# Optimization experiments

Hardware: AMD Instinct MI355X
Metric: run time of the kernel (lower is better)

Reference implementation:

```python
import jax, jax.numpy as jnp
import numpy as np

NUM_HEADS = 16

def setup_inputs() -> dict:
    key = jax.random.key(0)
    ks = jax.random.split(key, 7)
    B, S, D = 2, 2048, 1024
    X = jax.random.normal(ks[0], (B, S, D), dtype=jnp.float32)
    s = 1.0 / np.sqrt(D)
    Wq = jax.random.normal(ks[1], (D, D), dtype=jnp.float32) * s
    Wk = jax.random.normal(ks[2], (D, D), dtype=jnp.float32) * s
    Wv = jax.random.normal(ks[3], (D, D), dtype=jnp.float32) * s
    Wo = jax.random.normal(ks[4], (D, D), dtype=jnp.float32) * s
    bo = jnp.zeros((D,), dtype=jnp.float32)
    return {"X": X, "Wq": Wq, "Wk": Wk, "Wv": Wv, "Wo": Wo, "bo": bo}

def reference(X, Wq, Wk, Wv, Wo, bo):
    B, S, D = X.shape
    H = NUM_HEADS
    hd = D // H
    # project and split heads -> [B, H, S, hd]
    def split(t):
        return t.reshape(B, S, H, hd).transpose(0, 2, 1, 3)
    q = split(X @ Wq)
    k = split(X @ Wk)
    v = split(X @ Wv)
    scores = jnp.einsum('bhqd,bhkd->bhqk', q, k) / jnp.sqrt(jnp.float32(hd))
    causal = jnp.tril(jnp.ones((S, S), dtype=bool))
    scores = jnp.where(causal, scores, -jnp.inf)
    weights = jax.nn.softmax(scores, axis=-1)  # dropout p=0 -> identity
    ctx = jnp.einsum('bhqk,bhkd->bhqd', weights, v)
    ctx = ctx.transpose(0, 2, 1, 3).reshape(B, S, D)
    return ctx @ Wo + bo
```

## Files before the change

kernel.cpp:

```cpp
#include <hip/hip_runtime.h>


typedef __attribute__((ext_vector_type(8))) short short8;
typedef __attribute__((ext_vector_type(4))) short short4v;
typedef __attribute__((ext_vector_type(4))) float floatx4;

__device__ inline unsigned short f2bf(float f) {
  unsigned u = __float_as_uint(f);
  unsigned r = (u + 0x7fffu + ((u >> 16) & 1u)) >> 16;
  return (unsigned short)r;
}

__device__ __forceinline__ float fast_exp2(float x) {
#if __has_builtin(__builtin_amdgcn_exp2f)
  return __builtin_amdgcn_exp2f(x);
#else
  float r;
  asm volatile("v_exp_f32_e32 %0, %1" : "=v"(r) : "v"(x));
  return r;
#endif
}

__device__ __forceinline__ void gll16(const unsigned short* g, unsigned short* l) {
  __builtin_amdgcn_global_load_lds(
      (const __attribute__((address_space(1))) unsigned int*)(g),
      (__attribute__((address_space(3))) unsigned int*)(l),
      16, 0, 0);
}

constexpr int B_ = 2, S_ = 2048, D_ = 1024, H_ = 16, HD_ = 64;

__global__ __launch_bounds__(256) void prep_inputs(
    const float* __restrict__ x, unsigned short* __restrict__ xb,
    const float* __restrict__ w0, const float* __restrict__ w1,
    const float* __restrict__ w2, const float* __restrict__ w3,
    unsigned short* __restrict__ wt_base)
{
  if (blockIdx.z == 4) {
    const int tid = threadIdx.y * 32 + threadIdx.x;
    const size_t base =
        ((size_t)(blockIdx.y * 32 + blockIdx.x) * 256 + tid) * 16;
#pragma unroll
    for (int half = 0; half < 2; ++half) {
      const size_t i = base + half * 8;
      float4 a = *(const float4*)(x + i);
      float4 b = *(const float4*)(x + i + 4);
      short8 o;
      o[0] = (short)f2bf(a.x); o[1] = (short)f2bf(a.y);
      o[2] = (short)f2bf(a.z); o[3] = (short)f2bf(a.w);
      o[4] = (short)f2bf(b.x); o[5] = (short)f2bf(b.y);
      o[6] = (short)f2bf(b.z); o[7] = (short)f2bf(b.w);
      *(short8*)(xb + i) = o;
    }
    return;
  }
  const float* src;
  switch (blockIdx.z) {
    case 0: src = w0; break;
    case 1: src = w1; break;
    case 2: src = w2; break;
    default: src = w3; break;
  }
  unsigned short* dst = wt_base + (size_t)blockIdx.z * 1024 * 1024;
  __shared__ unsigned short t[32][33];
  const int bx = blockIdx.x * 32;
  const int by = blockIdx.y * 32;
  const int x_ = threadIdx.x;
  for (int yy = threadIdx.y; yy < 32; yy += 8)
    t[yy][x_] = f2bf(src[(size_t)(by + yy) * 1024 + bx + x_]);
  __syncthreads();
  for (int yy = threadIdx.y; yy < 32; yy += 8)
    dst[(size_t)(bx + yy) * 1024 + by + x_] = t[x_][yy];
}

__global__ __launch_bounds__(256) void gemm256_qkv(
    const unsigned short* __restrict__ A,
    const unsigned short* __restrict__ Bt,
    unsigned short* __restrict__ Qo,
    unsigned short* __restrict__ Ko,
    unsigned short* __restrict__ Vt)
{
  __shared__ unsigned short sA[2][128 * 32];
  __shared__ unsigned short sB[2][128 * 32];
  const int K = 1024;

  const int L = blockIdx.y * 24 + blockIdx.x;
  const int rid = (L & 7) * 96 + (L >> 3);
  const int brow = rid / 24, bcol = rid % 24;
  const int m0 = brow * 128;
  const int bn0 = bcol * 128;

  const int tid = threadIdx.x, wave = tid >> 6, lane = tid & 63;
  const int g = lane >> 4, ml = lane & 15;
  const int wm = wave & 1, wn = wave >> 1;

  const unsigned short* ag0 = A + (size_t)(m0 + (tid >> 2)) * K + (tid & 3) * 8;
  const unsigned short* ag1 = ag0 + (size_t)64 * K;
  const unsigned short* bg0 = Bt + (size_t)(bn0 + (tid >> 2)) * K + (tid & 3) * 8;
  const unsigned short* bg1 = bg0 + (size_t)64 * K;
  const int woff = wave * 512;

  floatx4 acc[4][4];
#pragma unroll
  for (int mt = 0; mt < 4; ++mt)
#pragma unroll
    for (int nt = 0; nt < 4; ++nt) acc[mt][nt] = (floatx4){0.f, 0.f, 0.f, 0.f};

  for (int k0 = 0; k0 < K; k0 += 64) {
    __syncthreads();
#pragma unroll
    for (int t = 0; t < 2; ++t) {
      gll16(ag0 + k0 + t * 32, sA[t] + woff);
      gll16(ag1 + k0 + t * 32, sA[t] + 2048 + woff);
      gll16(bg0 + k0 + t * 32, sB[t] + woff);
      gll16(bg1 + k0 + t * 32, sB[t] + 2048 + woff);
    }
    __syncthreads();
#pragma unroll
    for (int t = 0; t < 2; ++t) {
      short8 af[4], bf[4];
#pragma unroll
      for (int mt = 0; mt < 4; ++mt)
        af[mt] = *(const short8*)(sA[t] + (wm * 64 + mt * 16 + ml) * 32 + g * 8);
#pragma unroll
      for (int nt = 0; nt < 4; ++nt)
        bf[nt] = *(const short8*)(sB[t] + (wn * 64 + nt * 16 + ml) * 32 + g * 8);
#pragma unroll
      for (int mt = 0; mt < 4; ++mt)
#pragma unroll
        for (int nt = 0; nt < 4; ++nt)
          acc[mt][nt] = __builtin_amdgcn_mfma_f32_16x16x32_bf16(
              af[mt], bf[nt], acc[mt][nt], 0, 0, 0);
    }
  }

  const int proj = bcol >> 3;
  const int col0 = (bcol & 7) * 128;
  if (proj < 2) {
    unsigned short* out = (proj == 0) ? Qo : Ko;
#pragma unroll
    for (int mt = 0; mt < 4; ++mt) {
#pragma unroll
      for (int nt = 0; nt < 4; ++nt) {
        const int col = col0 + wn * 64 + nt * 16 + ml;
#pragma unroll
        for (int r = 0; r < 4; ++r) {
          const int row = m0 + wm * 64 + mt * 16 + g * 4 + r;
          out[(size_t)row * 1024 + col] = f2bf(acc[mt][nt][r]);
        }
      }
    }
  } else {
    const int bq = m0 >> 11;
    const int sbase = (m0 & 2047);
#pragma unroll
    for (int mt = 0; mt < 4; ++mt) {
      const int s0 = sbase + wm * 64 + mt * 16 + g * 4;
#pragma unroll
      for (int nt = 0; nt < 4; ++nt) {
        const int col = col0 + wn * 64 + nt * 16 + ml;
        const int h = col >> 6, d = col & 63;
        short4v o;
        o[0] = (short)f2bf(acc[mt][nt][0]);
        o[1] = (short)f2bf(acc[mt][nt][1]);
        o[2] = (short)f2bf(acc[mt][nt][2]);
        o[3] = (short)f2bf(acc[mt][nt][3]);
        *(short4v*)(Vt + ((size_t)((bq * 16 + h) * 64 + d)) * 2048 + s0) = o;
      }
    }
  }
}

__global__ __launch_bounds__(256) void gemm_wo64(
    const unsigned short* __restrict__ A,
    const unsigned short* __restrict__ Bt,
    const float* __restrict__ bias,
    float* __restrict__ C)
{
  __shared__ unsigned short sA[4][64 * 32];
  __shared__ unsigned short sB[4][128 * 32];
  const int K = 1024;

  const int L = blockIdx.y * 8 + blockIdx.x;
  const int rid = (L & 7) * 64 + (L >> 3);
  const int m0 = (rid >> 3) * 64;
  const int bn0 = (rid & 7) * 128;

  const int tid = threadIdx.x, wave = tid >> 6, lane = tid & 63;
  const int g = lane >> 4, ml = lane & 15;
  const int wm = wave & 1, wn = wave >> 1;

  const unsigned short* ag =
      A + (size_t)(m0 + wave * 16 + (lane >> 2)) * K + (lane & 3) * 8;
  const unsigned short* bg0 = Bt + (size_t)(bn0 + (tid >> 2)) * K + (tid & 3) * 8;
  const unsigned short* bg1 = bg0 + (size_t)64 * K;
  const int woff = wave * 512;

  floatx4 acc[2][4];
#pragma unroll
  for (int mt = 0; mt < 2; ++mt)
#pragma unroll
    for (int nt = 0; nt < 4; ++nt) acc[mt][nt] = (floatx4){0.f, 0.f, 0.f, 0.f};

  for (int k0 = 0; k0 < K; k0 += 128) {
    __syncthreads();
#pragma unroll
    for (int t = 0; t < 4; ++t) {
      gll16(ag + k0 + t * 32, sA[t] + woff);
      gll16(bg0 + k0 + t * 32, sB[t] + woff);
      gll16(bg1 + k0 + t * 32, sB[t] + 2048 + woff);
    }
    __syncthreads();
#pragma unroll
    for (int t = 0; t < 4; ++t) {
      short8 af[2], bf[4];
#pragma unroll
      for (int mt = 0; mt < 2; ++mt)
        af[mt] = *(const short8*)(sA[t] + (wm * 32 + mt * 16 + ml) * 32 + g * 8);
#pragma unroll
      for (int nt = 0; nt < 4; ++nt)
        bf[nt] = *(const short8*)(sB[t] + (wn * 64 + nt * 16 + ml) * 32 + g * 8);
#pragma unroll
      for (int mt = 0; mt < 2; ++mt)
#pragma unroll
        for (int nt = 0; nt < 4; ++nt)
          acc[mt][nt] = __builtin_amdgcn_mfma_f32_16x16x32_bf16(
              af[mt], bf[nt], acc[mt][nt], 0, 0, 0);
    }
  }

#pragma unroll
  for (int mt = 0; mt < 2; ++mt) {
#pragma unroll
    for (int nt = 0; nt < 4; ++nt) {
      const int col = bn0 + wn * 64 + nt * 16 + ml;
      const float badd = bias[col];
#pragma unroll
      for (int r = 0; r < 4; ++r) {
        const int row = m0 + wm * 32 + mt * 16 + g * 4 + r;
        C[(size_t)row * 1024 + col] = acc[mt][nt][r] + badd;
      }
    }
  }
}

constexpr int KTPB = 2;

struct AttnLds {
  unsigned short k0[2][KTPB][64 * 32];
  unsigned short k1[2][KTPB][64 * 32];
  unsigned short v0[2][KTPB][64 * 32];
  unsigned short v1[2][KTPB][64 * 32];
};
union __align__(16) AttnLdsU {
  AttnLds t;
  float comb[4 * 64 * 36];
};

__device__ __forceinline__ void softmax_pack(
    const floatx4* s, const bool diag, const int qg, const int kb,
    float& l, short8* ap)
{
  const float C1 = 0.18033688f;
  const float C2 = -34.6246810f;

  unsigned wb[4][4];
  float lp0 = 0.f, lp1 = 0.f, lp2 = 0.f, lp3 = 0.f;
#pragma unroll
  for (int nb = 0; nb < 4; ++nb) {
#pragma unroll
    for (int r = 0; r < 4; ++r) {
      float wv = fast_exp2(fmaf(s[nb][r], C1, C2));
      if (diag && (kb + nb * 16 + r > qg)) wv = 0.f;
      wb[nb][r] = __float_as_uint(wv);
      if (nb == 0) lp0 += wv;
      else if (nb == 1) lp1 += wv;
      else if (nb == 2) lp2 += wv;
      else lp3 += wv;
    }
  }
  l += (lp0 + lp1) + (lp2 + lp3);

  unsigned pk[4][2];
#pragma unroll
  for (int nb = 0; nb < 4; ++nb) {
    pk[nb][0] = __builtin_amdgcn_perm(wb[nb][1], wb[nb][0], 0x07060302u);
    pk[nb][1] = __builtin_amdgcn_perm(wb[nb][3], wb[nb][2], 0x07060302u);
  }

  unsigned Fr[2][4];
#pragma unroll
  for (int rr = 0; rr < 2; ++rr) {
    unsigned a0 = pk[0][rr], a1 = pk[1][rr];
    unsigned a2 = pk[2][rr], a3 = pk[3][rr];
    asm("v_permlane32_swap_b32 %0, %1" : "+v"(a0), "+v"(a1));
    asm("v_permlane32_swap_b32 %0, %1" : "+v"(a2), "+v"(a3));
    asm("v_permlane16_swap_b32 %0, %1" : "+v"(a0), "+v"(a1));
    asm("v_permlane16_swap_b32 %0, %1" : "+v"(a2), "+v"(a3));
    Fr[0][rr] = a0; Fr[0][2 + rr] = a1;
    Fr[1][rr] = a2; Fr[1][2 + rr] = a3;
  }
#pragma unroll
  for (int f = 0; f < 2; ++f) {
    union { unsigned u[4]; short8 s8; } uap;
    uap.u[0] = Fr[f][0]; uap.u[1] = Fr[f][1];
    uap.u[2] = Fr[f][2]; uap.u[3] = Fr[f][3];
    ap[f] = uap.s8;
  }
}

template <bool DUAL>
__device__ __forceinline__ void attn_tile2(
    const short8* aqB, const short8* aqA,
    const unsigned short* sK0, const unsigned short* sK1,
    const unsigned short* sV0, const unsigned short* sV1,
    floatx4* accB, float& lB, floatx4* accA, float& lA,
    const bool diagB, const bool diagA,
    const int qgB, const int qgA, const int kb,
    const int g, const int ml)
{
  floatx4 sB[4], sA[4];
  __builtin_amdgcn_s_setprio(1);
#pragma unroll
  for (int nb = 0; nb < 4; ++nb) {
    short8 bk0 = *(const short8*)(sK0 + (nb * 16 + ml) * 32 + g * 8);
    short8 bk1 = *(const short8*)(sK1 + (nb * 16 + ml) * 32 + g * 8);
    sB[nb] = (floatx4){0.f, 0.f, 0.f, 0.f};
    sB[nb] = __builtin_amdgcn_mfma_f32_16x16x32_bf16(bk0, aqB[0], sB[nb], 0, 0, 0);
    sB[nb] = __builtin_amdgcn_mfma_f32_16x16x32_bf16(bk1, aqB[1], sB[nb], 0, 0, 0);
    if (DUAL) {
      sA[nb] = (floatx4){0.f, 0.f, 0.f, 0.f};
      sA[nb] = __builtin_amdgcn_mfma_f32_16x16x32_bf16(bk0, aqA[0], sA[nb], 0, 0, 0);
      sA[nb] = __builtin_amdgcn_mfma_f32_16x16x32_bf16(bk1, aqA[1], sA[nb], 0, 0, 0);
    }
  }
  __builtin_amdgcn_s_setprio(0);

  short8 apB[2], apA[2];
  softmax_pack(sB, diagB, qgB, kb, lB, apB);
  if (DUAL) softmax_pack(sA, diagA, qgA, kb, lA, apA);

  __builtin_amdgcn_s_setprio(1);
#pragma unroll
  for (int f = 0; f < 2; ++f) {
    const unsigned short* sv = f ? sV1 : sV0;
#pragma unroll
    for (int jd = 0; jd < 4; ++jd) {
      short8 bv = *(const short8*)(sv + (jd * 16 + ml) * 32 + g * 8);
      accB[jd] = __builtin_amdgcn_mfma_f32_16x16x32_bf16(apB[f], bv, accB[jd], 0, 0, 0);
      if (DUAL)
        accA[jd] = __builtin_amdgcn_mfma_f32_16x16x32_bf16(apA[f], bv, accA[jd], 0, 0, 0);
    }
  }
  __builtin_amdgcn_s_setprio(0);
}

__global__ __launch_bounds__(512) void attn_v16(
    const unsigned short* __restrict__ Q,
    const unsigned short* __restrict__ Kg,
    const unsigned short* __restrict__ Vt,
    unsigned short* __restrict__ CTX)
{
  __shared__ AttnLdsU lds;

  const int L = blockIdx.x;
  const int rid = (L & 7) * 64 + (L >> 3);
  const int p = rid & 15;
  const int bh = rid >> 4;

  const int b = bh >> 4, h = bh & 15;
  const int qbA = p, qbB = 31 - p;
  const int qA0 = qbA * 64, qB0 = qbB * 64;
  const int tid = threadIdx.x, w = tid >> 6, lane = tid & 63;
  const int slice = w & 3, par = w >> 2;
  const int g = lane >> 4, ml = lane & 15;

  const size_t headoff = (size_t)b * S_ * D_ + (size_t)h * HD_;
  const size_t vtoff   = (size_t)bh * HD_ * S_;

  short8 aqA[2], aqB[2];
  {
    const unsigned short* qp =
        Q + headoff + (size_t)(qA0 + slice * 16 + ml) * D_ + g * 8;
    aqA[0] = *(const short8*)qp;
    aqA[1] = *(const short8*)(qp + 32);
  }
  {
    const unsigned short* qp =
        Q + headoff + (size_t)(qB0 + slice * 16 + ml) * D_ + g * 8;
    aqB[0] = *(const short8*)qp;
    aqB[1] = *(const short8*)(qp + 32);
  }

  floatx4 accA[4], accB[4];
#pragma unroll
  for (int jd = 0; jd < 4; ++jd) {
    accA[jd] = (floatx4){0.f, 0.f, 0.f, 0.f};
    accB[jd] = (floatx4){0.f, 0.f, 0.f, 0.f};
  }
  float lA = 0.f, lB = 0.f;
  const int qgA = qA0 + slice * 16 + ml;
  const int qgB = qB0 + slice * 16 + ml;

  const int sw = slice;
  const unsigned short* kgb =
      Kg + headoff + (size_t)(sw * 16 + (lane >> 2)) * D_ + (lane & 3) * 8;
  const unsigned short* vgb =
      Vt + vtoff + (size_t)(sw * 16 + (lane >> 2)) * S_ + (lane & 3) * 8;
  const int woff = sw * 512;

  const int ntiles = qbB + 1;

  {
    const int cnt = (ntiles < KTPB) ? ntiles : KTPB;
#pragma unroll
    for (int t = 0; t < KTPB; ++t) {
      if (t >= cnt) break;
      if (w < 4) {
        const size_t ko = (size_t)t * 64 * D_;
        gll16(kgb + ko,      lds.t.k0[0][t] + woff);
        gll16(kgb + ko + 32, lds.t.k1[0][t] + woff);
      } else {
        gll16(vgb + t * 64,      lds.t.v0[0][t] + woff);
        gll16(vgb + t * 64 + 32, lds.t.v1[0][t] + woff);
      }
    }
  }
  __syncthreads();

  for (int kt0 = 0; kt0 < ntiles; kt0 += KTPB) {
    const int bufi = (kt0 >> 1) & 1;
    const int nxt = kt0 + KTPB;
    if (nxt < ntiles) {
      const int cn = (ntiles - nxt < KTPB) ? (ntiles - nxt) : KTPB;
#pragma unroll
      for (int t = 0; t < KTPB; ++t) {
        if (t >= cn) break;
        const int kt = nxt + t;
        if (w < 4) {
          const size_t ko = (size_t)kt * 64 * D_;
          gll16(kgb + ko,      lds.t.k0[bufi ^ 1][t] + woff);
          gll16(kgb + ko + 32, lds.t.k1[bufi ^ 1][t] + woff);
        } else {
          gll16(vgb + kt * 64,      lds.t.v0[bufi ^ 1][t] + woff);
          gll16(vgb + kt * 64 + 32, lds.t.v1[bufi ^ 1][t] + woff);
        }
      }
    }

    const int cnt = (ntiles - kt0 < KTPB) ? (ntiles - kt0) : KTPB;
    if (par < cnt) {
      const int kt = kt0 + par;
      const int kb = kt * 64 + g * 4;
      if (kt <= qbA)
        attn_tile2<true>(aqB, aqA,
                         lds.t.k0[bufi][par], lds.t.k1[bufi][par],
                         lds.t.v0[bufi][par], lds.t.v1[bufi][par],
                         accB, lB, accA, lA,
                         kt == qbB, kt == qbA, qgB, qgA, kb, g, ml);
      else
        attn_tile2<false>(aqB, aqA,
                          lds.t.k0[bufi][par], lds.t.k1[bufi][par],
                          lds.t.v0[bufi][par], lds.t.v1[bufi][par],
                          accB, lB, accA, lA,
                          kt == qbB, false, qgB, qgA, kb, g, ml);
    }
    __syncthreads();
  }

  {
    float* slot = lds.comb + (size_t)(slice * 64 + lane) * 36;
    if (par == 1) {
#pragma unroll
      for (int jd = 0; jd < 4; ++jd) {
        *(floatx4*)(slot + jd * 4) = accA[jd];
        *(floatx4*)(slot + 16 + jd * 4) = accB[jd];
      }
      slot[32] = lA;
      slot[33] = lB;
    }
    __syncthreads();
    if (par == 1) return;
#pragma unroll
    for (int jd = 0; jd < 4; ++jd) {
      accA[jd] += *(const floatx4*)(slot + jd * 4);
      accB[jd] += *(const floatx4*)(slot + 16 + jd * 4);
    }
    lA += slot[32];
    lB += slot[33];
  }

  lA += __shfl_xor(lA, 16); lA += __shfl_xor(lA, 32);
  lB += __shfl_xor(lB, 16); lB += __shfl_xor(lB, 32);
  const float liA = 1.0f / lA;
  const float liB = 1.0f / lB;
  float lrA[4], lrB[4];
#pragma unroll
  for (int r = 0; r < 4; ++r) {
    lrA[r] = __shfl(liA, g * 4 + r);
    lrB[r] = __shfl(liB, g * 4 + r);
  }

#pragma unroll
  for (int r = 0; r < 4; ++r) {
    const int rowA = qA0 + slice * 16 + g * 4 + r;
    const int rowB = qB0 + slice * 16 + g * 4 + r;
#pragma unroll
    for (int jd = 0; jd < 4; ++jd) {
      CTX[headoff + (size_t)rowA * D_ + jd * 16 + ml] = f2bf(accA[jd][r] * lrA[r]);
      CTX[headoff + (size_t)rowB * D_ + jd * 16 + ml] = f2bf(accB[jd][r] * lrB[r]);
    }
  }
}

extern "C" void kernel_launch(void* const* d_in, const int* in_sizes, int n_in,
                              void* d_out, int out_size, void* d_ws, size_t ws_size,
                              hipStream_t stream)
{
  const float* X  = (const float*)d_in[0];
  const float* Wq = (const float*)d_in[1];
  const float* Wk = (const float*)d_in[2];
  const float* Wv = (const float*)d_in[3];
  const float* Wo = (const float*)d_in[4];
  const float* bo = (const float*)d_in[5];

  char* ws = (char*)d_ws;
  const size_t MB = 1024 * 1024;

  unsigned short* Qb  = (unsigned short*)(ws);
  unsigned short* Kb  = (unsigned short*)(ws + 8 * MB);
  unsigned short* Xb  = (unsigned short*)(ws + 16 * MB);
  unsigned short* WT  = (unsigned short*)(ws + 24 * MB);
  unsigned short* WoT = WT + (size_t)3 * 1024 * 1024;
  unsigned short* Vt  = (unsigned short*)d_out;

  prep_inputs<<<dim3(32, 32, 5), dim3(32, 8), 0, stream>>>(
      X, Xb, Wq, Wk, Wv, Wo, WT);
  gemm256_qkv<<<dim3(24, 32), 256, 0, stream>>>(Xb, WT, Qb, Kb, Vt);
  attn_v16<<<dim3(512), 512, 0, stream>>>(Qb, Kb, Vt, Qb);
  gemm_wo64<<<dim3(8, 64), 256, 0, stream>>>(Qb, WoT, bo, (float*)d_out);
}
```

Measured before the change: 188.1 us.

## Double-buffer LDS in projection GEMMs and remap QKV tiles per XCD

Both projection GEMMs now prefetch the next K-slice into a second LDS buffer with global_load_lds while the MFMAs consume the current one, so each step needs one barrier instead of two. This is meant to hide global load latency behind compute. The Wo GEMM's K-step drops from 128 to 64 so the double buffer fits in LDS. The QKV block-to-tile mapping is also changed so each XCD covers a contiguous 8x12 tile region, which should improve L2 reuse. The cost is doubled LDS use in the QKV kernel, which may lower occupancy, and it relies on the barrier at the end of each step to order the async LDS writes.

Result: slower. 195.4 us (+3.9%).

```diff
diff --git a/kernel.cpp b/kernel.cpp
--- a/kernel.cpp
+++ b/kernel.cpp
@@ -80,13 +80,14 @@
     unsigned short* __restrict__ Ko,
     unsigned short* __restrict__ Vt)
 {
-  __shared__ unsigned short sA[2][128 * 32];
-  __shared__ unsigned short sB[2][128 * 32];
+  __shared__ unsigned short sA[2][2][128 * 32];
+  __shared__ unsigned short sB[2][2][128 * 32];
   const int K = 1024;
 
   const int L = blockIdx.y * 24 + blockIdx.x;
-  const int rid = (L & 7) * 96 + (L >> 3);
-  const int brow = rid / 24, bcol = rid % 24;
+  const int xcd = L & 7, i = L >> 3;
+  const int brow = (xcd >> 1) * 8 + i / 12;
+  const int bcol = (xcd & 1) * 12 + i % 12;
   const int m0 = brow * 128;
   const int bn0 = bcol * 128;
 
@@ -106,25 +107,36 @@
 #pragma unroll
     for (int nt = 0; nt < 4; ++nt) acc[mt][nt] = (floatx4){0.f, 0.f, 0.f, 0.f};
 
-  for (int k0 = 0; k0 < K; k0 += 64) {
-    __syncthreads();
-#pragma unroll
-    for (int t = 0; t < 2; ++t) {
-      gll16(ag0 + k0 + t * 32, sA[t] + woff);
-      gll16(ag1 + k0 + t * 32, sA[t] + 2048 + woff);
-      gll16(bg0 + k0 + t * 32, sB[t] + woff);
-      gll16(bg1 + k0 + t * 32, sB[t] + 2048 + woff);
-    }
-    __syncthreads();
+#pragma unroll
+  for (int t = 0; t < 2; ++t) {
+    gll16(ag0 + t * 32, sA[0][t] + woff);
+    gll16(ag1 + t * 32, sA[0][t] + 2048 + woff);
+    gll16(bg0 + t * 32, sB[0][t] + woff);
+    gll16(bg1 + t * 32, sB[0][t] + 2048 + woff);
+  }
+  __syncthreads();
+
+  for (int k0 = 0, it = 0; k0 < K; k0 += 64, ++it) {
+    const int buf = it & 1;
+    const int kn = k0 + 64;
+    if (kn < K) {
+#pragma unroll
+      for (int t = 0; t < 2; ++t) {
+        gll16(ag0 + kn + t * 32, sA[buf ^ 1][t] + woff);
+        gll16(ag1 + kn + t * 32, sA[buf ^ 1][t] + 2048 + woff);
+        gll16(bg0 + kn + t * 32, sB[buf ^ 1][t] + woff);
+        gll16(bg1 + kn + t * 32, sB[buf ^ 1][t] + 2048 + woff);
+      }
+    }
 #pragma unroll
     for (int t = 0; t < 2; ++t) {
       short8 af[4], bf[4];
 #pragma unroll
       for (int mt = 0; mt < 4; ++mt)
-        af[mt] = *(const short8*)(sA[t] + (wm * 64 + mt * 16 + ml) * 32 + g * 8);
+        af[mt] = *(const short8*)(sA[buf][t] + (wm * 64 + mt * 16 + ml) * 32 + g * 8);
 #pragma unroll
       for (int nt = 0; nt < 4; ++nt)
-        bf[nt] = *(const short8*)(sB[t] + (wn * 64 + nt * 16 + ml) * 32 + g * 8);
+        bf[nt] = *(const short8*)(sB[buf][t] + (wn * 64 + nt * 16 + ml) * 32 + g * 8);
 #pragma unroll
       for (int mt = 0; mt < 4; ++mt)
 #pragma unroll
@@ -132,6 +144,7 @@
           acc[mt][nt] = __builtin_amdgcn_mfma_f32_16x16x32_bf16(
               af[mt], bf[nt], acc[mt][nt], 0, 0, 0);
     }
+    __syncthreads();
   }
 
   const int proj = bcol >> 3;
@@ -177,8 +190,8 @@
     const float* __restrict__ bias,
     float* __restrict__ C)
 {
-  __shared__ unsigned short sA[4][64 * 32];
-  __shared__ unsigned short sB[4][128 * 32];
+  __shared__ unsigned short sA[2][2][64 * 32];
+  __shared__ unsigned short sB[2][2][128 * 32];
   const int K = 1024;
 
   const int L = blockIdx.y * 8 + blockIdx.x;
@@ -202,24 +215,34 @@
 #pragma unroll
     for (int nt = 0; nt < 4; ++nt) acc[mt][nt] = (floatx4){0.f, 0.f, 0.f, 0.f};
 
-  for (int k0 = 0; k0 < K; k0 += 128) {
-    __syncthreads();
-#pragma unroll
-    for (int t = 0; t < 4; ++t) {
-      gll16(ag + k0 + t * 32, sA[t] + woff);
-      gll16(bg0 + k0 + t * 32, sB[t] + woff);
-      gll16(bg1 + k0 + t * 32, sB[t] + 2048 + woff);
-    }
-    __syncthreads();
-#pragma unroll
-    for (int t = 0; t < 4; ++t) {
+#pragma unroll
+  for (int t = 0; t < 2; ++t) {
+    gll16(ag + t * 32, sA[0][t] + woff);
+    gll16(bg0 + t * 32, sB[0][t] + woff);
+    gll16(bg1 + t * 32, sB[0][t] + 2048 + woff);
+  }
+  __syncthreads();
+
+  for (int k0 = 0, it = 0; k0 < K; k0 += 64, ++it) {
+    const int buf = it & 1;
+    const int kn = k0 + 64;
+    if (kn < K) {
+#pragma unroll
+      for (int t = 0; t < 2; ++t) {
+        gll16(ag + kn + t * 32, sA[buf ^ 1][t] + woff);
+        gll16(bg0 + kn + t * 32, sB[buf ^ 1][t] + woff);
+        gll16(bg1 + kn + t * 32, sB[buf ^ 1][t] + 2048 + woff);
+      }
+    }
+#pragma unroll
+    for (int t = 0; t < 2; ++t) {
       short8 af[2], bf[4];
 #pragma unroll
       for (int mt = 0; mt < 2; ++mt)
-        af[mt] = *(const short8*)(sA[t] + (wm * 32 + mt * 16 + ml) * 32 + g * 8);
+        af[mt] = *(const short8*)(sA[buf][t] + (wm * 32 + mt * 16 + ml) * 32 + g * 8);
 #pragma unroll
       for (int nt = 0; nt < 4; ++nt)
-        bf[nt] = *(const short8*)(sB[t] + (wn * 64 + nt * 16 + ml) * 32 + g * 8);
+        bf[nt] = *(const short8*)(sB[buf][t] + (wn * 64 + nt * 16 + ml) * 32 + g * 8);
 #pragma unroll
       for (int mt = 0; mt < 2; ++mt)
 #pragma unroll
@@ -227,6 +250,7 @@
           acc[mt][nt] = __builtin_amdgcn_mfma_f32_16x16x32_bf16(
               af[mt], bf[nt], acc[mt][nt], 0, 0, 0);
     }
+    __syncthreads();
   }
 
 #pragma unroll
```
